# Optimization experiments

Measured on AMD Instinct MI355X. Metric: run time of the kernel, lower is better.

Reference implementation:

```python
import jax, jax.numpy as jnp
import numpy as np

N_NODES = 100000
N_FEAT = 128
HIDDEN = 64
OUT = 16
N_EDGES = 3200000
N_POS = 500000
N_NEG = 500000


def setup_inputs() -> dict:
    key = jax.random.key(0)
    ks = jax.random.split(key, 8)
    x = jax.random.normal(ks[0], (N_NODES, N_FEAT), dtype=jnp.float32)
    edge_index = jax.random.randint(ks[1], (2, N_EDGES), 0, N_NODES, dtype=jnp.int64)
    pos_edge_index = jax.random.randint(ks[2], (2, N_POS), 0, N_NODES, dtype=jnp.int64)
    neg_edge_index = jax.random.randint(ks[3], (2, N_NEG), 0, N_NODES, dtype=jnp.int64)
    W1 = jax.random.normal(ks[4], (N_FEAT, HIDDEN), dtype=jnp.float32) * (1.0 / np.sqrt(N_FEAT))
    b1 = jnp.zeros((HIDDEN,), dtype=jnp.float32)
    W2 = jax.random.normal(ks[5], (HIDDEN, OUT), dtype=jnp.float32) * (1.0 / np.sqrt(HIDDEN))
    b2 = jnp.zeros((OUT,), dtype=jnp.float32)
    return {"x": x, "edge_index": edge_index, "pos_edge_index": pos_edge_index,
            "neg_edge_index": neg_edge_index, "W1": W1, "b1": b1, "W2": W2, "b2": b2}


def gcn_conv(x, W, b, src, dst):
    """PyG GCNConv with add_self_loops=True: D^-1/2 (A+I) D^-1/2 X W + b."""
    n = x.shape[0]
    h = x @ W  # [N, out]
    # degree including self-loop (+1)
    deg = jax.ops.segment_sum(jnp.ones(dst.shape, dtype=h.dtype), dst, num_segments=n) + 1.0
    dis = jax.lax.rsqrt(deg)  # deg >= 1, never inf
    coef = dis[src] * dis[dst]  # [E]
    agg = jax.ops.segment_sum(h[src] * coef[:, None], dst, num_segments=n)
    # self-loop message: norm = dis[i]*dis[i]
    agg = agg + h * (dis * dis)[:, None]
    return agg + b


def reference(x, edge_index, pos_edge_index, neg_edge_index, W1, b1, W2, b2):
    src, dst = edge_index[0], edge_index[1]
    z = jax.nn.relu(gcn_conv(x, W1, b1, src, dst))
    z = gcn_conv(z, W2, b2, src, dst)  # [N, 16]
    ei = jnp.concatenate([pos_edge_index, neg_edge_index], axis=-1)  # [2, P+Q]
    logits = jnp.sum(z[ei[0]] * z[ei[1]], axis=-1)  # [P+Q]
    return logits
```

## Files before the change

### kernel.cpp

```cpp
#include <hip/hip_runtime.h>

#define F 128
#define H 64
#define O 16

#define BSHIFT 7
#define BSZ 128
#define NSUB 16
#define SUBCAP 384
#define ACHUNK 8192
#define XS 136

typedef _Float16 half8_t __attribute__((ext_vector_type(8)));
typedef _Float16 half4_t __attribute__((ext_vector_type(4)));
typedef float f32x4 __attribute__((ext_vector_type(4)));

#define MIX2(alo, ahi, dw)                                                              \
    do {                                                                                \
        asm("v_fma_mix_f32 %0, %1, 1.0, %0 op_sel_hi:[1,0,0]"                           \
            : "+v"(alo) : "v"(dw));                                                     \
        asm("v_fma_mix_f32 %0, %1, 1.0, %0 op_sel:[1,0,0] op_sel_hi:[1,0,0]"            \
            : "+v"(ahi) : "v"(dw));                                                     \
    } while (0)

#define MIXROW(r)                                                                       \
    do {                                                                                \
        MIX2(acc[0], acc[1], (r).x);                                                    \
        MIX2(acc[2], acc[3], (r).y);                                                    \
        MIX2(acc[4], acc[5], (r).z);                                                    \
        MIX2(acc[6], acc[7], (r).w);                                                    \
    } while (0)

__global__ void k_prep(const float* __restrict__ W1, _Float16* __restrict__ wt_hi,
                       _Float16* __restrict__ wt_lo, int* __restrict__ bcur, int NC) {
    int i = blockIdx.x * blockDim.x + threadIdx.x;
    if (i < NC) bcur[i] = i * SUBCAP;
    if (i < H * F) {
        int c = i >> 7, k = i & 127;
        float w = W1[k * H + c];
        _Float16 hi = (_Float16)w;
        wt_hi[i] = hi;
        wt_lo[i] = (_Float16)(w - (float)hi);
    }
}

__global__ __launch_bounds__(512) void k_bucketA(const int* __restrict__ src,
                                                 const int* __restrict__ dstv,
                                                 int* __restrict__ bcur,
                                                 int* __restrict__ bdata, int E) {
    __shared__ int hist[1024];
    for (int t = threadIdx.x; t < 1024; t += 512) hist[t] = 0;
    __syncthreads();
    int base = blockIdx.x * ACHUNK;
    int end = min(base + ACHUNK, E);
    int tid = threadIdx.x;
    int4 s4r[4], d4r[4];
    bool ok[4];
#pragma unroll
    for (int k = 0; k < 4; k++) {
        int i = base + tid * 4 + k * 2048;
        ok[k] = (i + 3 < end);
        if (ok[k]) {
            d4r[k] = *(const int4*)(dstv + i);
            s4r[k] = *(const int4*)(src + i);
            atomicAdd(&hist[d4r[k].x >> BSHIFT], 1);
            atomicAdd(&hist[d4r[k].y >> BSHIFT], 1);
            atomicAdd(&hist[d4r[k].z >> BSHIFT], 1);
            atomicAdd(&hist[d4r[k].w >> BSHIFT], 1);
        }
    }
    for (int i = base + ((end - base) & ~3) + tid; i < end; i += 512)
        atomicAdd(&hist[dstv[i] >> BSHIFT], 1);
    __syncthreads();
    int sub = blockIdx.x & (NSUB - 1);
    for (int b = tid; b < 1024; b += 512) {
        int c = hist[b];
        if (c > 0) hist[b] = atomicAdd(&bcur[b * NSUB + sub], c);
    }
    __syncthreads();
#pragma unroll
    for (int k = 0; k < 4; k++) {
        if (ok[k]) {
            int4 s4 = s4r[k];
            int4 d4 = d4r[k];
            int p0 = atomicAdd(&hist[d4.x >> BSHIFT], 1);
            bdata[p0] = (s4.x << BSHIFT) | (d4.x & (BSZ - 1));
            int p1 = atomicAdd(&hist[d4.y >> BSHIFT], 1);
            bdata[p1] = (s4.y << BSHIFT) | (d4.y & (BSZ - 1));
            int p2 = atomicAdd(&hist[d4.z >> BSHIFT], 1);
            bdata[p2] = (s4.z << BSHIFT) | (d4.z & (BSZ - 1));
            int p3 = atomicAdd(&hist[d4.w >> BSHIFT], 1);
            bdata[p3] = (s4.w << BSHIFT) | (d4.w & (BSZ - 1));
        }
    }
    for (int i = base + ((end - base) & ~3) + tid; i < end; i += 512) {
        int d = dstv[i];
        int pos = atomicAdd(&hist[d >> BSHIFT], 1);
        bdata[pos] = (src[i] << BSHIFT) | (d & (BSZ - 1));
    }
}

__global__ __launch_bounds__(256) void k_bplace(const int* __restrict__ bdata,
                                                const int* __restrict__ bcur,
                                                int* __restrict__ row_ptr,
                                                float* __restrict__ dis,
                                                int* __restrict__ col, int N) {
    __shared__ int h[BSZ];
    __shared__ int pref[BSZ];
    __shared__ int cur[BSZ];
    __shared__ int red[256];
    int b = blockIdx.x;
    int node0 = b << BSHIFT;
    int nloc = min(BSZ, N - node0);
    int tid = threadIdx.x;
    int partial = 0;
    int limit = b * NSUB;
    for (int i = tid; i < limit; i += 256)
        partial += bcur[i] - i * SUBCAP;
    red[tid] = partial;
    if (tid < BSZ) h[tid] = 0;
    __syncthreads();
    for (int off = 128; off > 0; off >>= 1) {
        if (tid < off) red[tid] += red[tid + off];
        __syncthreads();
    }
    int base = red[0];
    for (int s = 0; s < NSUB; s++) {
        int start = (b * NSUB + s) * SUBCAP;
        int end = bcur[b * NSUB + s];
        for (int p = start + tid; p < end; p += 256)
            atomicAdd(&h[bdata[p] & (BSZ - 1)], 1);
    }
    __syncthreads();
    int myDeg = 0;
    if (tid < BSZ) {
        myDeg = h[tid];
        pref[tid] = myDeg;
    }
    __syncthreads();
    for (int off = 1; off < BSZ; off <<= 1) {
        int v = (tid < BSZ && tid >= off) ? pref[tid - off] : 0;
        __syncthreads();
        if (tid < BSZ) pref[tid] += v;
        __syncthreads();
    }
    if (tid < nloc) {
        int excl = base + pref[tid] - myDeg;
        cur[tid] = excl;
        row_ptr[node0 + tid] = excl;
        dis[node0 + tid] = rsqrtf((float)myDeg + 1.0f);
    }
    if (tid == 0) row_ptr[node0 + nloc] = base + pref[BSZ - 1];
    __syncthreads();
    for (int s = 0; s < NSUB; s++) {
        int start = (b * NSUB + s) * SUBCAP;
        int end = bcur[b * NSUB + s];
        for (int p = start + tid; p < end; p += 256) {
            int v = bdata[p];
            int pos = atomicAdd(&cur[v & (BSZ - 1)], 1);
            col[pos] = v >> BSHIFT;
        }
    }
}

__global__ __launch_bounds__(256) void k_gemm1(const float* __restrict__ x,
                                               const _Float16* __restrict__ wt_hi,
                                               const _Float16* __restrict__ wt_lo,
                                               const float* __restrict__ dis,
                                               _Float16* __restrict__ h1p, int N) {
    __shared__ _Float16 xh[64 * XS], xl[64 * XS], wh[64 * XS], wl[64 * XS];
    int tid = threadIdx.x;
    int row0 = blockIdx.x * 64;
#pragma unroll
    for (int i = 0; i < 8; i++) {
        int idx = i * 256 + tid;
        int r = idx >> 5;
        int c = (idx & 31) * 4;
        int rr = row0 + r; if (rr >= N) rr = N - 1;
        float4 v = *(const float4*)(x + (size_t)rr * F + c);
        half4_t h = {(_Float16)v.x, (_Float16)v.y, (_Float16)v.z, (_Float16)v.w};
        half4_t l = {(_Float16)(v.x - (float)h[0]), (_Float16)(v.y - (float)h[1]),
                     (_Float16)(v.z - (float)h[2]), (_Float16)(v.w - (float)h[3])};
        *(half4_t*)(xh + r * XS + c) = h;
        *(half4_t*)(xl + r * XS + c) = l;
    }
#pragma unroll
    for (int i = 0; i < 4; i++) {
        int idx = i * 256 + tid;
        int c = idx >> 4;
        int k8 = (idx & 15) * 8;
        *(half8_t*)(wh + c * XS + k8) = *(const half8_t*)(wt_hi + c * 128 + k8);
        *(half8_t*)(wl + c * XS + k8) = *(const half8_t*)(wt_lo + c * 128 + k8);
    }
    __syncthreads();
    int wv = tid >> 6, lane = tid & 63;
    int m = lane & 15, qd = lane >> 4;
    const _Float16* xhp = xh + (wv * 16 + m) * XS;
    const _Float16* xlp = xl + (wv * 16 + m) * XS;
    f32x4 acc[4] = {f32x4{0,0,0,0}, f32x4{0,0,0,0}, f32x4{0,0,0,0}, f32x4{0,0,0,0}};
#pragma unroll
    for (int kc = 0; kc < 4; kc++) {
        int ko = kc * 32 + qd * 8;
        half8_t ah = *(const half8_t*)(xhp + ko);
        half8_t al = *(const half8_t*)(xlp + ko);
#pragma unroll
        for (int nt = 0; nt < 4; nt++) {
            half8_t bh = *(const half8_t*)(wh + (nt * 16 + m) * XS + ko);
            half8_t bl = *(const half8_t*)(wl + (nt * 16 + m) * XS + ko);
            acc[nt] = __builtin_amdgcn_mfma_f32_16x16x32_f16(ah, bh, acc[nt], 0, 0, 0);
            acc[nt] = __builtin_amdgcn_mfma_f32_16x16x32_f16(ah, bl, acc[nt], 0, 0, 0);
            acc[nt] = __builtin_amdgcn_mfma_f32_16x16x32_f16(al, bh, acc[nt], 0, 0, 0);
        }
    }
#pragma unroll
    for (int reg = 0; reg < 4; reg++) {
        int row = row0 + wv * 16 + qd * 4 + reg;
        if (row < N) {
            float d = dis[row];
#pragma unroll
            for (int nt = 0; nt < 4; nt++) {
                h1p[(size_t)row * H + nt * 16 + m] = (_Float16)(acc[nt][reg] * d);
            }
        }
    }
}

__global__ __launch_bounds__(256) void k_gather1(const _Float16* __restrict__ h1p,
                                                 const float* __restrict__ dis,
                                                 const int* __restrict__ row_ptr,
                                                 const int* __restrict__ col,
                                                 const float* __restrict__ b1,
                                                 const float* __restrict__ W2,
                                                 _Float16* __restrict__ h2p, int N) {
    __shared__ float w2t[16 * 65];
    int tid = threadIdx.x;
    {
        int idx = tid * 4;
        float4 v = *(const float4*)(W2 + idx);
        const float* vp = (const float*)&v;
#pragma unroll
        for (int i = 0; i < 4; i++) {
            int e = idx + i;
            w2t[(e & 15) * 65 + (e >> 4)] = vp[i];
        }
    }
    __syncthreads();
    int lane = tid & 63;
    int h = lane >> 5;
    int g2 = (lane >> 3) & 3;
    int g = lane >> 3;
    int t = lane & 7;
    unsigned t16 = (unsigned)t * 16;
    const char* hb = (const char*)h1p;
    int hsign = 1 - 2 * h;
    float bb[8];
#pragma unroll
    for (int j = 0; j < 8; j++) bb[j] = b1[t * 8 + j];
    float w1v[8], w2v[8];
#pragma unroll
    for (int j = 0; j < 8; j++) {
        w1v[j] = w2t[g * 65 + t * 8 + j];
        w2v[j] = w2t[(g + 8) * 65 + t * 8 + j];
    }

    int stride = gridDim.x * 8;
    int node = blockIdx.x * 8 + (tid >> 6) * 2 + h;
    int rpA = 0, rpB = 0;
    if (node < N) { rpA = row_ptr[node]; rpB = row_ptr[node + 1]; }
    while (node < N) {
        int nnode = node + stride;
        int nA = 0, nB = 0;
        if (nnode < N) { nA = row_ptr[nnode]; nB = row_ptr[nnode + 1]; }
        float acc[8];
#pragma unroll
        for (int j = 0; j < 8; j++) acc[j] = 0.f;
        int e = rpB;
        int p = rpA + g2;
        for (; p + 28 < e; p += 32) {
            int s0 = col[p],      s1 = col[p + 4],  s2 = col[p + 8],  s3 = col[p + 12];
            int s4 = col[p + 16], s5 = col[p + 20], s6 = col[p + 24], s7 = col[p + 28];
            int4 r0 = *(const int4*)(hb + (((unsigned)s0 << 7) + t16));
            int4 r1 = *(const int4*)(hb + (((unsigned)s1 << 7) + t16));
            int4 r2 = *(const int4*)(hb + (((unsigned)s2 << 7) + t16));
            int4 r3 = *(const int4*)(hb + (((unsigned)s3 << 7) + t16));
            int4 r4 = *(const int4*)(hb + (((unsigned)s4 << 7) + t16));
            int4 r5 = *(const int4*)(hb + (((unsigned)s5 << 7) + t16));
            int4 r6 = *(const int4*)(hb + (((unsigned)s6 << 7) + t16));
            int4 r7 = *(const int4*)(hb + (((unsigned)s7 << 7) + t16));
            MIXROW(r0); MIXROW(r1); MIXROW(r2); MIXROW(r3);
            MIXROW(r4); MIXROW(r5); MIXROW(r6); MIXROW(r7);
        }
        for (; p + 12 < e; p += 16) {
            int s0 = col[p], s1 = col[p + 4], s2 = col[p + 8], s3 = col[p + 12];
            int4 r0 = *(const int4*)(hb + (((unsigned)s0 << 7) + t16));
            int4 r1 = *(const int4*)(hb + (((unsigned)s1 << 7) + t16));
            int4 r2 = *(const int4*)(hb + (((unsigned)s2 << 7) + t16));
            int4 r3 = *(const int4*)(hb + (((unsigned)s3 << 7) + t16));
            MIXROW(r0); MIXROW(r1); MIXROW(r2); MIXROW(r3);
        }
        for (; p + 4 < e; p += 8) {
            int s0 = col[p], s1 = col[p + 4];
            int4 r0 = *(const int4*)(hb + (((unsigned)s0 << 7) + t16));
            int4 r1 = *(const int4*)(hb + (((unsigned)s1 << 7) + t16));
            MIXROW(r0); MIXROW(r1);
        }
        if (p < e) {
            int s0 = col[p];
            int4 r0 = *(const int4*)(hb + (((unsigned)s0 << 7) + t16));
            MIXROW(r0);
        }
        if (g2 == 0) {
            int4 rs = *(const int4*)(hb + (((unsigned)node << 7) + t16));
            MIXROW(rs);
        }
#pragma unroll
        for (int off = 8; off < 32; off <<= 1) {
#pragma unroll
            for (int j = 0; j < 8; j++) acc[j] += __shfl_xor(acc[j], off);
        }
        float dn = dis[node];
        float o[8];
#pragma unroll
        for (int j = 0; j < 8; j++)
            o[j] = fmaxf(fmaf(acc[j], dn, bb[j]), 0.f);
        float oo[8];
#pragma unroll
        for (int j = 0; j < 8; j++) oo[j] = __shfl_xor(o[j], 32);
        float dno = __shfl_xor(dn, 32);
        float p1o = 0.f, p2o = 0.f, p1x = 0.f, p2x = 0.f;
#pragma unroll
        for (int j = 0; j < 8; j++) {
            p1o = fmaf(o[j], w1v[j], p1o);
            p2o = fmaf(o[j], w2v[j], p2o);
            p1x = fmaf(oo[j], w1v[j], p1x);
            p2x = fmaf(oo[j], w2v[j], p2x);
        }
#pragma unroll
        for (int off = 1; off < 8; off <<= 1) {
            p1o += __shfl_xor(p1o, off);
            p2o += __shfl_xor(p2o, off);
            p1x += __shfl_xor(p1x, off);
            p2x += __shfl_xor(p2x, off);
        }
        if (t == 0) {
            h2p[(size_t)node * O + g]     = (_Float16)(p1o * dn);
            h2p[(size_t)node * O + g + 8] = (_Float16)(p2o * dn);
            int nodeo = node + hsign;
            if (nodeo < N) {
                h2p[(size_t)nodeo * O + g]     = (_Float16)(p1x * dno);
                h2p[(size_t)nodeo * O + g + 8] = (_Float16)(p2x * dno);
            }
        }
        node = nnode; rpA = nA; rpB = nB;
    }
}

__global__ __launch_bounds__(256) void k_gather2(const _Float16* __restrict__ h2p,
                                                 const float* __restrict__ dis,
                                                 const int* __restrict__ row_ptr,
                                                 const int* __restrict__ col,
                                                 const float* __restrict__ b2,
                                                 float* __restrict__ z2, int N) {
    int tid = threadIdx.x;
    int lane = tid & 63;
    int g = lane >> 1;
    int t = lane & 1;
    unsigned t16 = (unsigned)t * 16;
    const char* hb = (const char*)h2p;
    float bb[8];
#pragma unroll
    for (int j = 0; j < 8; j++) bb[j] = b2[t * 8 + j];

    for (int node = blockIdx.x * 4 + (tid >> 6); node < N; node += gridDim.x * 4) {
        float acc[8];
#pragma unroll
        for (int j = 0; j < 8; j++) acc[j] = 0.f;
        int e = row_ptr[node + 1];
        for (int p = row_ptr[node] + g; p < e; p += 32) {
            int s = col[p];
            int4 r = *(const int4*)(hb + (((unsigned)s << 5) + t16));
            MIXROW(r);
        }
        if (g == 0) {
            int4 rs = *(const int4*)(hb + (((unsigned)node << 5) + t16));
            MIXROW(rs);
        }
#pragma unroll
        for (int off = 2; off < 64; off <<= 1) {
#pragma unroll
            for (int j = 0; j < 8; j++) acc[j] += __shfl_xor(acc[j], off);
        }
        if (g == 0) {
            float dn = dis[node];
            float o[8];
#pragma unroll
            for (int j = 0; j < 8; j++)
                o[j] = fmaf(acc[j], dn, bb[j]);
            float4* zp = (float4*)(z2 + (size_t)node * O + t * 8);
            zp[0] = float4{o[0], o[1], o[2], o[3]};
            zp[1] = float4{o[4], o[5], o[6], o[7]};
        }
    }
}

__global__ __launch_bounds__(256) void k_logits(const float* __restrict__ z2,
                                                const int* __restrict__ pos,
                                                const int* __restrict__ neg,
                                                float* __restrict__ out, int P, int Q) {
    int tid = blockIdx.x * 256 + threadIdx.x;
    int i = tid >> 2;
    if (i >= P + Q) return;
    int k = tid & 3;
    unsigned k16 = (unsigned)k * 16;
    const char* zb = (const char*)z2;
    int a, b;
    if (i < P) { a = pos[i]; b = pos[P + i]; }
    else       { int t = i - P; a = neg[t]; b = neg[Q + t]; }
    float4 va = *(const float4*)(zb + (((unsigned)a << 6) + k16));
    float4 vb = *(const float4*)(zb + (((unsigned)b << 6) + k16));
    float r = va.x * vb.x + va.y * vb.y + va.z * vb.z + va.w * vb.w;
    r += __shfl_xor(r, 1);
    r += __shfl_xor(r, 2);
    if (k == 0) out[i] = r;
}

extern "C" void kernel_launch(void* const* d_in, const int* in_sizes, int n_in,
                              void* d_out, int out_size, void* d_ws, size_t ws_size,
                              hipStream_t stream) {
    const float* x   = (const float*)d_in[0];
    const int*   ei  = (const int*)d_in[1];
    const int*   pos = (const int*)d_in[2];
    const int*   neg = (const int*)d_in[3];
    const float* W1  = (const float*)d_in[4];
    const float* b1  = (const float*)d_in[5];
    const float* W2  = (const float*)d_in[6];
    const float* b2  = (const float*)d_in[7];
    float* out = (float*)d_out;

    int N = in_sizes[0] / F;
    int E = in_sizes[1] / 2;
    int P = in_sizes[2] / 2;
    int Q = in_sizes[3] / 2;
    const int* src  = ei;
    const int* dstv = ei + E;

    int Npad = ((N + 255) / 256) * 256;
    int Epad = (E + 63) & ~63;
    int NBK = (N + BSZ - 1) / BSZ;
    int NC  = NBK * NSUB;

    char* w = (char*)d_ws;
    float*    dis     = (float*)w;    w += (size_t)Npad * 4;
    int*      row_ptr = (int*)w;      w += (size_t)(Npad + 256) * 4;
    int*      bcur    = (int*)w;      w += 16384 * 4;
    int*      col     = (int*)w;      w += (size_t)Epad * 4;
    _Float16* h1p     = (_Float16*)w;
    int*      bdata   = (int*)w;
    size_t h1b = (size_t)N * H * 2, bdb = (size_t)NC * SUBCAP * 4;
    w += (h1b > bdb ? h1b : bdb);
    _Float16* h2p     = (_Float16*)w; w += (size_t)N * O * 2;
    float*    z2      = (float*)w;    w += (size_t)N * O * 4;
    _Float16* wt_hi   = (_Float16*)w; w += (size_t)H * F * 2;
    _Float16* wt_lo   = (_Float16*)w;

    int prepN = (NC > H * F) ? NC : H * F;

    k_prep<<<(prepN + 255) / 256, 256, 0, stream>>>(W1, wt_hi, wt_lo, bcur, NC);
    k_bucketA<<<(E + ACHUNK - 1) / ACHUNK, 512, 0, stream>>>(src, dstv, bcur, bdata, E);
    k_bplace<<<NBK, 256, 0, stream>>>(bdata, bcur, row_ptr, dis, col, N);

    k_gemm1<<<(N + 63) / 64, 256, 0, stream>>>(x, wt_hi, wt_lo, dis, h1p, N);
    k_gather1<<<2048, 256, 0, stream>>>(h1p, dis, row_ptr, col, b1, W2, h2p, N);
    k_gather2<<<(N + 3) / 4, 256, 0, stream>>>(h2p, dis, row_ptr, col, b2, z2, N);
    k_logits<<<((P + Q) * 4 + 255) / 256, 256, 0, stream>>>(z2, pos, neg, out, P, Q);
}
```

Measured before the change: 307.2 us.

## Sort CSR neighbors into source-range quarters and interleave gather1 across four nodes

The CSR build now splits each node's neighbor list into four sub-ranges by the high bits of the source index and records the four boundaries in a new per-node int4 array. gather1 processes four nodes per wave concurrently, sweeping the first source quarter for all four nodes, then the second, and so on. The aim is to keep concurrent gathers within a narrower region of h1 for better cache locality, and to expose more independent loads. It costs extra LDS histogram bins, one more per-node int4 write and read, more registers for four accumulators, and a fixed four-node-per-thread coverage (4096 blocks times GSTRIDE) that replaces the old grid-stride loop.

```diff
diff --git a/kernel.cpp b/kernel.cpp
--- a/kernel.cpp
+++ b/kernel.cpp
@@ -10,6 +10,7 @@
 #define SUBCAP 384
 #define ACHUNK 8192
 #define XS 136
+#define GSTRIDE 32768
 
 typedef _Float16 half8_t __attribute__((ext_vector_type(8)));
 typedef _Float16 half4_t __attribute__((ext_vector_type(4)));
@@ -23,12 +24,12 @@
             : "+v"(ahi) : "v"(dw));                                                     \
     } while (0)
 
-#define MIXROW(r)                                                                       \
+#define MIXROW8(A, r)                                                                   \
     do {                                                                                \
-        MIX2(acc[0], acc[1], (r).x);                                                    \
-        MIX2(acc[2], acc[3], (r).y);                                                    \
-        MIX2(acc[4], acc[5], (r).z);                                                    \
-        MIX2(acc[6], acc[7], (r).w);                                                    \
+        MIX2(A[0], A[1], (r).x);                                                        \
+        MIX2(A[2], A[3], (r).y);                                                        \
+        MIX2(A[4], A[5], (r).z);                                                        \
+        MIX2(A[6], A[7], (r).w);                                                        \
     } while (0)
 
 __global__ void k_prep(const float* __restrict__ W1, _Float16* __restrict__ wt_hi,
@@ -104,10 +105,11 @@
                                                 const int* __restrict__ bcur,
                                                 int* __restrict__ row_ptr,
                                                 float* __restrict__ dis,
+                                                int4* __restrict__ bp4,
                                                 int* __restrict__ col, int N) {
-    __shared__ int h[BSZ];
+    __shared__ int hb[BSZ * 4];
     __shared__ int pref[BSZ];
-    __shared__ int cur[BSZ];
+    __shared__ int cur[BSZ * 4];
     __shared__ int red[256];
     int b = blockIdx.x;
     int node0 = b << BSHIFT;
@@ -118,7 +120,7 @@
     for (int i = tid; i < limit; i += 256)
         partial += bcur[i] - i * SUBCAP;
     red[tid] = partial;
-    if (tid < BSZ) h[tid] = 0;
+    hb[tid] = 0; hb[tid + 256] = 0;
     __syncthreads();
     for (int off = 128; off > 0; off >>= 1) {
         if (tid < off) red[tid] += red[tid + off];
@@ -128,13 +130,15 @@
     for (int s = 0; s < NSUB; s++) {
         int start = (b * NSUB + s) * SUBCAP;
         int end = bcur[b * NSUB + s];
-        for (int p = start + tid; p < end; p += 256)
-            atomicAdd(&h[bdata[p] & (BSZ - 1)], 1);
+        for (int p = start + tid; p < end; p += 256) {
+            int v = bdata[p];
+            atomicAdd(&hb[((v & (BSZ - 1)) << 2) | (v >> 22)], 1);
+        }
     }
     __syncthreads();
     int myDeg = 0;
     if (tid < BSZ) {
-        myDeg = h[tid];
+        myDeg = hb[tid << 2] + hb[(tid << 2) | 1] + hb[(tid << 2) | 2] + hb[(tid << 2) | 3];
         pref[tid] = myDeg;
     }
     __syncthreads();
@@ -146,8 +150,16 @@
     }
     if (tid < nloc) {
         int excl = base + pref[tid] - myDeg;
-        cur[tid] = excl;
+        int c0 = excl;
+        int c1 = c0 + hb[tid << 2];
+        int c2 = c1 + hb[(tid << 2) | 1];
+        int c3 = c2 + hb[(tid << 2) | 2];
+        cur[tid << 2]       = c0;
+        cur[(tid << 2) | 1] = c1;
+        cur[(tid << 2) | 2] = c2;
+        cur[(tid << 2) | 3] = c3;
         row_ptr[node0 + tid] = excl;
+        bp4[node0 + tid] = int4{c0, c1, c2, c3};
         dis[node0 + tid] = rsqrtf((float)myDeg + 1.0f);
     }
     if (tid == 0) row_ptr[node0 + nloc] = base + pref[BSZ - 1];
@@ -157,7 +169,7 @@
         int end = bcur[b * NSUB + s];
         for (int p = start + tid; p < end; p += 256) {
             int v = bdata[p];
-            int pos = atomicAdd(&cur[v & (BSZ - 1)], 1);
+            int pos = atomicAdd(&cur[((v & (BSZ - 1)) << 2) | (v >> 22)], 1);
             col[pos] = v >> BSHIFT;
         }
     }
@@ -228,6 +240,7 @@
 __global__ __launch_bounds__(256) void k_gather1(const _Float16* __restrict__ h1p,
                                                  const float* __restrict__ dis,
                                                  const int* __restrict__ row_ptr,
+                                                 const int4* __restrict__ bp4,
                                                  const int* __restrict__ col,
                                                  const float* __restrict__ b1,
                                                  const float* __restrict__ W2,
@@ -251,107 +264,117 @@
     int g = lane >> 3;
     int t = lane & 7;
     unsigned t16 = (unsigned)t * 16;
-    const char* hb = (const char*)h1p;
+    const char* hbp = (const char*)h1p;
     int hsign = 1 - 2 * h;
     float bb[8];
 #pragma unroll
     for (int j = 0; j < 8; j++) bb[j] = b1[t * 8 + j];
-    float w1v[8], w2v[8];
-#pragma unroll
-    for (int j = 0; j < 8; j++) {
-        w1v[j] = w2t[g * 65 + t * 8 + j];
-        w2v[j] = w2t[(g + 8) * 65 + t * 8 + j];
-    }
-
-    int stride = gridDim.x * 8;
-    int node = blockIdx.x * 8 + (tid >> 6) * 2 + h;
-    int rpA = 0, rpB = 0;
-    if (node < N) { rpA = row_ptr[node]; rpB = row_ptr[node + 1]; }
-    while (node < N) {
-        int nnode = node + stride;
-        int nA = 0, nB = 0;
-        if (nnode < N) { nA = row_ptr[nnode]; nB = row_ptr[nnode + 1]; }
-        float acc[8];
-#pragma unroll
-        for (int j = 0; j < 8; j++) acc[j] = 0.f;
-        int e = rpB;
-        int p = rpA + g2;
-        for (; p + 28 < e; p += 32) {
-            int s0 = col[p],      s1 = col[p + 4],  s2 = col[p + 8],  s3 = col[p + 12];
-            int s4 = col[p + 16], s5 = col[p + 20], s6 = col[p + 24], s7 = col[p + 28];
-            int4 r0 = *(const int4*)(hb + (((unsigned)s0 << 7) + t16));
-            int4 r1 = *(const int4*)(hb + (((unsigned)s1 << 7) + t16));
-            int4 r2 = *(const int4*)(hb + (((unsigned)s2 << 7) + t16));
-            int4 r3 = *(const int4*)(hb + (((unsigned)s3 << 7) + t16));
-            int4 r4 = *(const int4*)(hb + (((unsigned)s4 << 7) + t16));
-            int4 r5 = *(const int4*)(hb + (((unsigned)s5 << 7) + t16));
-            int4 r6 = *(const int4*)(hb + (((unsigned)s6 << 7) + t16));
-            int4 r7 = *(const int4*)(hb + (((unsigned)s7 << 7) + t16));
-            MIXROW(r0); MIXROW(r1); MIXROW(r2); MIXROW(r3);
-            MIXROW(r4); MIXROW(r5); MIXROW(r6); MIXROW(r7);
-        }
-        for (; p + 12 < e; p += 16) {
-            int s0 = col[p], s1 = col[p + 4], s2 = col[p + 8], s3 = col[p + 12];
-            int4 r0 = *(const int4*)(hb + (((unsigned)s0 << 7) + t16));
-            int4 r1 = *(const int4*)(hb + (((unsigned)s1 << 7) + t16));
-            int4 r2 = *(const int4*)(hb + (((unsigned)s2 << 7) + t16));
-            int4 r3 = *(const int4*)(hb + (((unsigned)s3 << 7) + t16));
-            MIXROW(r0); MIXROW(r1); MIXROW(r2); MIXROW(r3);
-        }
-        for (; p + 4 < e; p += 8) {
-            int s0 = col[p], s1 = col[p + 4];
-            int4 r0 = *(const int4*)(hb + (((unsigned)s0 << 7) + t16));
-            int4 r1 = *(const int4*)(hb + (((unsigned)s1 << 7) + t16));
-            MIXROW(r0); MIXROW(r1);
-        }
-        if (p < e) {
-            int s0 = col[p];
-            int4 r0 = *(const int4*)(hb + (((unsigned)s0 << 7) + t16));
-            MIXROW(r0);
-        }
-        if (g2 == 0) {
-            int4 rs = *(const int4*)(hb + (((unsigned)node << 7) + t16));
-            MIXROW(rs);
-        }
-#pragma unroll
-        for (int off = 8; off < 32; off <<= 1) {
-#pragma unroll
-            for (int j = 0; j < 8; j++) acc[j] += __shfl_xor(acc[j], off);
-        }
-        float dn = dis[node];
-        float o[8];
-#pragma unroll
-        for (int j = 0; j < 8; j++)
-            o[j] = fmaxf(fmaf(acc[j], dn, bb[j]), 0.f);
-        float oo[8];
-#pragma unroll
-        for (int j = 0; j < 8; j++) oo[j] = __shfl_xor(o[j], 32);
-        float dno = __shfl_xor(dn, 32);
-        float p1o = 0.f, p2o = 0.f, p1x = 0.f, p2x = 0.f;
-#pragma unroll
-        for (int j = 0; j < 8; j++) {
-            p1o = fmaf(o[j], w1v[j], p1o);
-            p2o = fmaf(o[j], w2v[j], p2o);
-            p1x = fmaf(oo[j], w1v[j], p1x);
-            p2x = fmaf(oo[j], w2v[j], p2x);
-        }
-#pragma unroll
-        for (int off = 1; off < 8; off <<= 1) {
-            p1o += __shfl_xor(p1o, off);
-            p2o += __shfl_xor(p2o, off);
-            p1x += __shfl_xor(p1x, off);
-            p2x += __shfl_xor(p2x, off);
-        }
-        if (t == 0) {
-            h2p[(size_t)node * O + g]     = (_Float16)(p1o * dn);
-            h2p[(size_t)node * O + g + 8] = (_Float16)(p2o * dn);
-            int nodeo = node + hsign;
-            if (nodeo < N) {
-                h2p[(size_t)nodeo * O + g]     = (_Float16)(p1x * dno);
-                h2p[(size_t)nodeo * O + g + 8] = (_Float16)(p2x * dno);
+    const float* w1r = w2t + g * 65 + t * 8;
+    const float* w2r = w2t + (g + 8) * 65 + t * 8;
+
+    int nbase = blockIdx.x * 8 + (tid >> 6) * 2 + h;
+    int4 bpv[4];
+    int ev[4];
+    float acc[4][8];
+#pragma unroll
+    for (int it = 0; it < 4; it++) {
+        int node = nbase + it * GSTRIDE;
+#pragma unroll
+        for (int j = 0; j < 8; j++) acc[it][j] = 0.f;
+        if (node < N) {
+            bpv[it] = bp4[node];
+            ev[it] = row_ptr[node + 1];
+        } else {
+            bpv[it] = int4{0, 0, 0, 0};
+            ev[it] = 0;
+        }
+    }
+
+#define EDGELOOP(IT, PS, PE)                                                            \
+    {                                                                                   \
+        int p = (PS) + g2, pe = (PE);                                                   \
+        for (; p + 4 < pe; p += 8) {                                                    \
+            int s0 = col[p], s1 = col[p + 4];                                           \
+            int4 r0 = *(const int4*)(hbp + (((unsigned)s0 << 7) + t16));                \
+            int4 r1 = *(const int4*)(hbp + (((unsigned)s1 << 7) + t16));                \
+            MIXROW8(acc[IT], r0);                                                       \
+            MIXROW8(acc[IT], r1);                                                       \
+        }                                                                               \
+        if (p < pe) {                                                                   \
+            int s0 = col[p];                                                            \
+            int4 r0 = *(const int4*)(hbp + (((unsigned)s0 << 7) + t16));                \
+            MIXROW8(acc[IT], r0);                                                       \
+        }                                                                               \
+    }
+
+    EDGELOOP(0, bpv[0].x, bpv[0].y)
+    EDGELOOP(1, bpv[1].x, bpv[1].y)
+    EDGELOOP(2, bpv[2].x, bpv[2].y)
+    EDGELOOP(3, bpv[3].x, bpv[3].y)
+    EDGELOOP(0, bpv[0].y, bpv[0].z)
+    EDGELOOP(1, bpv[1].y, bpv[1].z)
+    EDGELOOP(2, bpv[2].y, bpv[2].z)
+    EDGELOOP(3, bpv[3].y, bpv[3].z)
+    EDGELOOP(0, bpv[0].z, bpv[0].w)
+    EDGELOOP(1, bpv[1].z, bpv[1].w)
+    EDGELOOP(2, bpv[2].z, bpv[2].w)
+    EDGELOOP(3, bpv[3].z, bpv[3].w)
+    EDGELOOP(0, bpv[0].w, ev[0])
+    EDGELOOP(1, bpv[1].w, ev[1])
+    EDGELOOP(2, bpv[2].w, ev[2])
+    EDGELOOP(3, bpv[3].w, ev[3])
+#undef EDGELOOP
+
+#pragma unroll
+    for (int it = 0; it < 4; it++) {
+        int node = nbase + it * GSTRIDE;
+        if (node < N) {
+            float a[8];
+#pragma unroll
+            for (int j = 0; j < 8; j++) a[j] = acc[it][j];
+            if (g2 == 0) {
+                int4 rs = *(const int4*)(hbp + (((unsigned)node << 7) + t16));
+                MIXROW8(a, rs);
             }
-        }
-        node = nnode; rpA = nA; rpB = nB;
+#pragma unroll
+            for (int off = 8; off < 32; off <<= 1) {
+#pragma unroll
+                for (int j = 0; j < 8; j++) a[j] += __shfl_xor(a[j], off);
+            }
+            float dn = dis[node];
+            float o[8];
+#pragma unroll
+            for (int j = 0; j < 8; j++)
+                o[j] = fmaxf(fmaf(a[j], dn, bb[j]), 0.f);
+            float oo[8];
+#pragma unroll
+            for (int j = 0; j < 8; j++) oo[j] = __shfl_xor(o[j], 32);
+            float dno = __shfl_xor(dn, 32);
+            float p1o = 0.f, p2o = 0.f, p1x = 0.f, p2x = 0.f;
+#pragma unroll
+            for (int j = 0; j < 8; j++) {
+                p1o = fmaf(o[j], w1r[j], p1o);
+                p2o = fmaf(o[j], w2r[j], p2o);
+                p1x = fmaf(oo[j], w1r[j], p1x);
+                p2x = fmaf(oo[j], w2r[j], p2x);
+            }
+#pragma unroll
+            for (int off = 1; off < 8; off <<= 1) {
+                p1o += __shfl_xor(p1o, off);
+                p2o += __shfl_xor(p2o, off);
+                p1x += __shfl_xor(p1x, off);
+                p2x += __shfl_xor(p2x, off);
+            }
+            if (t == 0) {
+                h2p[(size_t)node * O + g]     = (_Float16)(p1o * dn);
+                h2p[(size_t)node * O + g + 8] = (_Float16)(p2o * dn);
+                int nodeo = node + hsign;
+                if (nodeo < N) {
+                    h2p[(size_t)nodeo * O + g]     = (_Float16)(p1x * dno);
+                    h2p[(size_t)nodeo * O + g + 8] = (_Float16)(p2x * dno);
+                }
+            }
+        }
     }
 }
 
@@ -379,11 +402,11 @@
         for (int p = row_ptr[node] + g; p < e; p += 32) {
             int s = col[p];
             int4 r = *(const int4*)(hb + (((unsigned)s << 5) + t16));
-            MIXROW(r);
+            MIXROW8(acc, r);
         }
         if (g == 0) {
             int4 rs = *(const int4*)(hb + (((unsigned)node << 5) + t16));
-            MIXROW(rs);
+            MIXROW8(acc, rs);
         }
 #pragma unroll
         for (int off = 2; off < 64; off <<= 1) {
@@ -461,16 +484,17 @@
     _Float16* h2p     = (_Float16*)w; w += (size_t)N * O * 2;
     float*    z2      = (float*)w;    w += (size_t)N * O * 4;
     _Float16* wt_hi   = (_Float16*)w; w += (size_t)H * F * 2;
-    _Float16* wt_lo   = (_Float16*)w;
+    _Float16* wt_lo   = (_Float16*)w; w += (size_t)H * F * 2;
+    int4*     bp4     = (int4*)w;     w += (size_t)Npad * 16;
 
     int prepN = (NC > H * F) ? NC : H * F;
 
     k_prep<<<(prepN + 255) / 256, 256, 0, stream>>>(W1, wt_hi, wt_lo, bcur, NC);
     k_bucketA<<<(E + ACHUNK - 1) / ACHUNK, 512, 0, stream>>>(src, dstv, bcur, bdata, E);
-    k_bplace<<<NBK, 256, 0, stream>>>(bdata, bcur, row_ptr, dis, col, N);
+    k_bplace<<<NBK, 256, 0, stream>>>(bdata, bcur, row_ptr, dis, bp4, col, N);
 
     k_gemm1<<<(N + 63) / 64, 256, 0, stream>>>(x, wt_hi, wt_lo, dis, h1p, N);
-    k_gather1<<<2048, 256, 0, stream>>>(h1p, dis, row_ptr, col, b1, W2, h2p, N);
+    k_gather1<<<4096, 256, 0, stream>>>(h1p, dis, row_ptr, bp4, col, b1, W2, h2p, N);
     k_gather2<<<(N + 3) / 4, 256, 0, stream>>>(h2p, dis, row_ptr, col, b2, z2, N);
     k_logits<<<((P + Q) * 4 + 255) / 256, 256, 0, stream>>>(z2, pos, neg, out, P, Q);
 }
```

After: 345.0 us. 12.3% more time.
